# Kernel tuning notes

Hardware: AMD Instinct MI355X
Metric: run time of the kernel (lower is better)

Reference implementation:

```python
import jax, jax.numpy as jnp
import numpy as np

B, T, C = 1, 2048, 1024
H, KVH = 16, 4
D = C // H            # 64
KV = KVH * D          # 256
EPS = 1e-6
SCALE = 1.0 / np.sqrt(D)
ROPE_BASE = 10000.0


def setup_inputs() -> dict:
    key = jax.random.key(0)
    ks = jax.random.split(key, 8)
    s = 0.02
    return dict(
        x=jax.random.normal(ks[0], (B, T, C), jnp.float32),
        Wq=jax.random.normal(ks[1], (C, C), jnp.float32) * s,
        Wk=jax.random.normal(ks[2], (KV, C), jnp.float32) * s,
        Wv=jax.random.normal(ks[3], (KV, C), jnp.float32) * s,
        Wo=jax.random.normal(ks[4], (C, C), jnp.float32) * s,
        q_norm_w=jnp.ones((C,), jnp.float32),
        k_norm_w=jnp.ones((KV,), jnp.float32),
        fgate_w=jax.random.normal(ks[5], (H, C), jnp.float32) * s,
        fgate_b=jnp.zeros((H,), jnp.float32),
        weight_lambda=jax.random.normal(ks[6], (C, H), jnp.float32) * s,
    )


def _rmsnorm(x, w):
    var = jnp.mean(x * x, axis=-1, keepdims=True)
    return x * jax.lax.rsqrt(var + EPS) * w


def _rotate_half(x):
    x1, x2 = jnp.split(x, 2, axis=-1)
    return jnp.concatenate([-x2, x1], axis=-1)


def _apply_rope(q, k):
    # q: [B,H,T,D], k: [B,KVH,T,D]; position_ids = arange(T)
    inv_freq = 1.0 / (ROPE_BASE ** (jnp.arange(0, D, 2, dtype=jnp.float32) / D))
    freqs = jnp.outer(jnp.arange(T, dtype=jnp.float32), inv_freq)  # [T, D/2]
    emb = jnp.concatenate([freqs, freqs], axis=-1)                 # [T, D]
    cos = jnp.cos(emb)[None, None]                                  # [1,1,T,D]
    sin = jnp.sin(emb)[None, None]
    return q * cos + _rotate_half(q) * sin, k * cos + _rotate_half(k) * sin


def _forward(x, Wq, Wk, Wv, Wo, q_norm_w, k_norm_w, fgate_w, fgate_b, weight_lambda):
    q = _rmsnorm(x @ Wq.T, q_norm_w)          # [B,T,C]
    k = _rmsnorm(x @ Wk.T, k_norm_w)          # [B,T,KV]
    v = x @ Wv.T                              # [B,T,KV]
    q = q.reshape(B, T, H, D).transpose(0, 2, 1, 3)     # [B,H,T,D]
    k = k.reshape(B, T, KVH, D).transpose(0, 2, 1, 3)   # [B,KVH,T,D]
    v = v.reshape(B, T, KVH, D).transpose(0, 2, 1, 3)
    q, k = _apply_rope(q, k)
    # GQA: repeat_interleave kv heads
    g = H // KVH
    k = jnp.repeat(k, g, axis=1)              # [B,H,T,D]
    v = jnp.repeat(v, g, axis=1)
    # Forgetting gate (FoX): log f_t per head, with elu-based lambda scaling
    lam = jax.nn.elu(x @ weight_lambda) + 1.0            # [B,T,H]
    logit = (x @ fgate_w.T + fgate_b) * lam              # [B,T,H]
    log_f = (jax.nn.log_sigmoid(logit) / (lam + 1e-3)).transpose(0, 2, 1)  # [B,H,T]
    c = jnp.cumsum(log_f, axis=-1)                       # [B,H,T]
    bias = c[..., :, None] - c[..., None, :]             # [B,H,T,T]: sum_{t=j+1..i} log f_t
    scores = jnp.einsum('bhid,bhjd->bhij', q, k) * SCALE + bias
    causal = jnp.tril(jnp.ones((T, T), dtype=bool))
    scores = jnp.where(causal, scores, -jnp.inf)
    p = jax.nn.softmax(scores, axis=-1)
    y = jnp.einsum('bhij,bhjd->bhid', p, v)              # [B,H,T,D]
    y = y.transpose(0, 2, 1, 3).reshape(B, T, C)
    return y @ Wo.T


def reference(x, Wq, Wk, Wv, Wo, q_norm_w, k_norm_w, fgate_w, fgate_b, weight_lambda):
    return _forward(x, Wq, Wk, Wv, Wo, q_norm_w, k_norm_w, fgate_w, fgate_b, weight_lambda)
```

## Files before the change

kernel.cpp:

```cpp
#include <hip/hip_runtime.h>

typedef __bf16 bf16x8 __attribute__((ext_vector_type(8)));
typedef float f32x4 __attribute__((ext_vector_type(4)));

#define MFMA_BF16 __builtin_amdgcn_mfma_f32_16x16x32_bf16

static constexpr int T_ = 2048;
static constexpr int C_ = 1024;
static constexpr int H_ = 16;
static constexpr int KVH_ = 4;
static constexpr int D_ = 64;
static constexpr float SCALE_ = 0.125f;
static constexpr float MSHIFT_ = 10.0f;

__device__ inline void cvt8(__bf16* dst, const float* src) {
  float4 a = *(const float4*)src;
  float4 b = *(const float4*)(src + 4);
  bf16x8 r;
  r[0] = (__bf16)a.x; r[1] = (__bf16)a.y; r[2] = (__bf16)a.z; r[3] = (__bf16)a.w;
  r[4] = (__bf16)b.x; r[5] = (__bf16)b.y; r[6] = (__bf16)b.z; r[7] = (__bf16)b.w;
  *(bf16x8*)dst = r;
}

__global__ __launch_bounds__(256) void cvt_kernel(
    const float* __restrict__ x,  const float* __restrict__ wq,
    const float* __restrict__ wk, const float* __restrict__ wv,
    const float* __restrict__ wo, const float* __restrict__ wl,
    __bf16* __restrict__ xb,  __bf16* __restrict__ wqb,
    __bf16* __restrict__ wkb, __bf16* __restrict__ wvb,
    __bf16* __restrict__ wob, float* __restrict__ wlT)
{
  size_t i8 = ((size_t)blockIdx.x * 256 + threadIdx.x) * 8;
  if (i8 < 2097152)       cvt8(xb  + i8,            x  + i8);
  else if (i8 < 3145728)  cvt8(wqb + (i8-2097152),  wq + (i8-2097152));
  else if (i8 < 3407872)  cvt8(wkb + (i8-3145728),  wk + (i8-3145728));
  else if (i8 < 3670016)  cvt8(wvb + (i8-3407872),  wv + (i8-3407872));
  else if (i8 < 4718592)  cvt8(wob + (i8-3670016),  wo + (i8-3670016));
  else {
    size_t r = i8 - 4718592;
    if (r < 16384) {
#pragma unroll
      for (int j = 0; j < 8; ++j) {
        size_t idx = r + j;
        size_t hh = idx >> 10, c = idx & 1023;
        wlT[idx] = wl[c * 16 + hh];
      }
    }
  }
}

template <int BM>
__global__ __launch_bounds__(256) void gemm_bt_kernel(
    const __bf16* __restrict__ A, int K, int N,
    const __bf16* __restrict__ B0, int e0,
    const __bf16* __restrict__ B1, int e1,
    const __bf16* __restrict__ B2,
    float* __restrict__ outF)
{
  __shared__ __bf16 la[BM * 40];
  __shared__ __bf16 lb[128 * 40];
  const int m0 = blockIdx.y * BM;
  const int n0 = blockIdx.x * 128;
  const __bf16* Bs; int nrel;
  if (n0 < e0)      { Bs = B0; nrel = n0; }
  else if (n0 < e1) { Bs = B1; nrel = n0 - e0; }
  else              { Bs = B2; nrel = n0 - e1; }
  const int tid = threadIdx.x;
  const int arow = tid >> 2, acol = (tid & 3) * 8;
  const __bf16* ap = A  + (size_t)(m0   + arow) * K + acol;
  const __bf16* bp = Bs + (size_t)(nrel + arow) * K + acol;
  const int w = tid >> 6, lane = tid & 63, lq = lane >> 4, ln = lane & 15;
  const int wm = (w >> 1) * (BM / 2), wn = (w & 1) * 64;
  constexpr int FM = BM / 32;
  f32x4 acc[FM][4] = {};
  for (int k0 = 0; k0 < K; k0 += 32) {
    bf16x8 a0 = *(const bf16x8*)(ap + k0);
    bf16x8 a1{};
    if (BM == 128) a1 = *(const bf16x8*)(ap + (size_t)64 * K + k0);
    bf16x8 b0 = *(const bf16x8*)(bp + k0);
    bf16x8 b1 = *(const bf16x8*)(bp + (size_t)64 * K + k0);
    __syncthreads();
    *(bf16x8*)(la + arow * 40 + acol) = a0;
    if (BM == 128) *(bf16x8*)(la + (arow + 64) * 40 + acol) = a1;
    *(bf16x8*)(lb + arow * 40 + acol) = b0;
    *(bf16x8*)(lb + (arow + 64) * 40 + acol) = b1;
    __syncthreads();
    bf16x8 af[FM], bfr[4];
#pragma unroll
    for (int i = 0; i < FM; ++i)
      af[i] = *(const bf16x8*)(la + (wm + i * 16 + ln) * 40 + lq * 8);
#pragma unroll
    for (int j = 0; j < 4; ++j)
      bfr[j] = *(const bf16x8*)(lb + (wn + j * 16 + ln) * 40 + lq * 8);
#pragma unroll
    for (int i = 0; i < FM; ++i)
#pragma unroll
      for (int j = 0; j < 4; ++j)
        acc[i][j] = MFMA_BF16(af[i], bfr[j], acc[i][j], 0, 0, 0);
  }
#pragma unroll
  for (int i = 0; i < FM; ++i)
#pragma unroll
    for (int j = 0; j < 4; ++j)
#pragma unroll
      for (int r = 0; r < 4; ++r) {
        int row = m0 + wm + i * 16 + lq * 4 + r;
        int col = n0 + wn + j * 16 + ln;
        outF[(size_t)row * N + col] = acc[i][j][r];
      }
}

__global__ __launch_bounds__(256) void gates_kernel(
    const float* __restrict__ x, const float* __restrict__ fw,
    const float* __restrict__ fb, const float* __restrict__ wlT,
    float* __restrict__ logf)
{
  const int t = blockIdx.x;
  const int tid = threadIdx.x, w = tid >> 6, lane = tid & 63;
  float xv[16];
#pragma unroll
  for (int i = 0; i < 16; ++i)
    xv[i] = x[(size_t)t * C_ + i * 64 + lane];
#pragma unroll
  for (int u = 0; u < 4; ++u) {
    int h = w * 4 + u;
    float s1 = 0.f, s2 = 0.f;
#pragma unroll
    for (int i = 0; i < 16; ++i) {
      int cidx = i * 64 + lane;
      s1 += xv[i] * wlT[(size_t)h * C_ + cidx];
      s2 += xv[i] * fw[(size_t)h * C_ + cidx];
    }
    for (int m = 32; m; m >>= 1) {
      s1 += __shfl_xor(s1, m);
      s2 += __shfl_xor(s2, m);
    }
    if (lane == 0) {
      float lam = (s1 > 0.f ? s1 : expm1f(s1)) + 1.0f;
      float logit = (s2 + fb[h]) * lam;
      float ls = (logit >= 0.f) ? -log1pf(expf(-logit))
                                : (logit - log1pf(expf(logit)));
      logf[(size_t)h * T_ + t] = ls / (lam + 1e-3f);
    }
  }
}

__global__ __launch_bounds__(64) void cumsum_kernel(
    const float* __restrict__ logf, float* __restrict__ csum)
{
  const int h = blockIdx.x;
  const int lane = threadIdx.x;
  float carry = 0.f;
  for (int ch = 0; ch < T_ / 64; ++ch) {
    float v = logf[(size_t)h * T_ + ch * 64 + lane];
#pragma unroll
    for (int d = 1; d < 64; d <<= 1) {
      float tv = __shfl_up(v, d);
      if (lane >= d) v += tv;
    }
    v += carry;
    csum[(size_t)h * T_ + ch * 64 + lane] = v;
    carry = __shfl(v, 63);
  }
}

__global__ __launch_bounds__(256) void normrope_kernel(
    const float* __restrict__ qkv, const float* __restrict__ qw,
    const float* __restrict__ kw, __bf16* __restrict__ qh,
    __bf16* __restrict__ kh, __bf16* __restrict__ vh)
{
  const int t = blockIdx.x, tid = threadIdx.x;
  __shared__ float qn[1024];
  __shared__ float kn[256];
  __shared__ float red[16];
  __shared__ float rc[32], rs[32];
  if (tid < 32) {
    float fr = (float)t * exp2f((float)tid * -0.41524101186404527f);
    float sn, cs;
    sincosf(fr, &sn, &cs);
    rc[tid] = cs; rs[tid] = sn;
  }
  const float* row = qkv + (size_t)t * 1536;
  float4 q4 = *(const float4*)(row + tid * 4);
  float kvl = row[1024 + tid];
  float vvl = row[1280 + tid];
  float ssq = q4.x * q4.x + q4.y * q4.y + q4.z * q4.z + q4.w * q4.w;
  float ssk = kvl * kvl;
  const int lane = tid & 63, w = tid >> 6;
  for (int m = 32; m; m >>= 1) {
    ssq += __shfl_xor(ssq, m);
    ssk += __shfl_xor(ssk, m);
  }
  if (lane == 0) { red[w] = ssq; red[8 + w] = ssk; }
  __syncthreads();
  float sq = red[0] + red[1] + red[2] + red[3];
  float sk = red[8] + red[9] + red[10] + red[11];
  float rq = rsqrtf(sq * (1.0f / 1024.f) + 1e-6f);
  float rk = rsqrtf(sk * (1.0f / 256.f) + 1e-6f);
  qn[tid * 4 + 0] = q4.x * rq * qw[tid * 4 + 0];
  qn[tid * 4 + 1] = q4.y * rq * qw[tid * 4 + 1];
  qn[tid * 4 + 2] = q4.z * rq * qw[tid * 4 + 2];
  qn[tid * 4 + 3] = q4.w * rq * qw[tid * 4 + 3];
  kn[tid] = kvl * rk * kw[tid];
  __syncthreads();
#pragma unroll
  for (int u = 0; u < 4; ++u) {
    int cidx = tid * 4 + u;
    int hh = cidx >> 6, d = cidx & 63, i = d & 31;
    float cs = rc[i], sn = rs[i];
    float val = (d < 32) ? (qn[cidx] * cs - qn[cidx + 32] * sn)
                         : (qn[cidx] * cs + qn[cidx - 32] * sn);
    qh[(size_t)hh * T_ * D_ + (size_t)t * D_ + d] = (__bf16)val;
  }
  {
    int d = tid & 63, kvhh = tid >> 6, i = d & 31;
    float cs = rc[i], sn = rs[i];
    float kval = (d < 32) ? (kn[tid] * cs - kn[tid + 32] * sn)
                          : (kn[tid] * cs + kn[tid - 32] * sn);
    kh[(size_t)kvhh * T_ * D_ + (size_t)t * D_ + d] = (__bf16)kval;
    vh[(size_t)kvhh * T_ * D_ + (size_t)t * D_ + d] = (__bf16)vvl;
  }
}

__global__ __launch_bounds__(256) void vtrans_kernel(
    const __bf16* __restrict__ vh, __bf16* __restrict__ vt)
{
  const int tb = blockIdx.x, kvh = blockIdx.y;
  __shared__ __bf16 tile[64][72];
  const int tid = threadIdx.x;
  const int r = tid >> 2, cb = (tid & 3) * 16;
  const __bf16* src = vh + (size_t)kvh * T_ * D_ + (size_t)(tb * 64 + r) * D_ + cb;
  bf16x8 v0 = *(const bf16x8*)(src);
  bf16x8 v1 = *(const bf16x8*)(src + 8);
  *(bf16x8*)(&tile[r][cb]) = v0;
  *(bf16x8*)(&tile[r][cb + 8]) = v1;
  __syncthreads();
  bf16x8 o0, o1;
#pragma unroll
  for (int j = 0; j < 8; ++j) o0[j] = tile[cb + j][r];
#pragma unroll
  for (int j = 0; j < 8; ++j) o1[j] = tile[cb + 8 + j][r];
  __bf16* dst = vt + (size_t)kvh * D_ * T_ + (size_t)r * T_ + tb * 64 + cb;
  *(bf16x8*)(dst) = o0;
  *(bf16x8*)(dst + 8) = o1;
}

__global__ __launch_bounds__(256) void attn_kernel(
    const __bf16* __restrict__ qh, const __bf16* __restrict__ kh,
    const __bf16* __restrict__ vt, const float* __restrict__ csum,
    __bf16* __restrict__ y)
{
  const int ib = blockIdx.x, h = blockIdx.y;
  const int i0 = ib * 64, kvh = h >> 2;
  __shared__ __bf16 kt[64 * 72];
  __shared__ __bf16 vtt[64 * 72];
  __shared__ __bf16 pt[4][16 * 72];
  const int tid = threadIdx.x;
  const int w = tid >> 6, lane = tid & 63, lq = lane >> 4, ln = lane & 15;
  const int srow = tid >> 2, scol = (tid & 3) * 16;
  const __bf16* kbase = kh + (size_t)kvh * T_ * D_;
  const __bf16* vbase = vt + (size_t)kvh * D_ * T_;
  const __bf16* qp = qh + ((size_t)h * T_ + i0 + w * 16 + ln) * D_;
  bf16x8 aq0 = *(const bf16x8*)(qp + lq * 8);
  bf16x8 aq1 = *(const bf16x8*)(qp + 32 + lq * 8);
  float ci[4];
#pragma unroll
  for (int r = 0; r < 4; ++r)
    ci[r] = csum[(size_t)h * T_ + i0 + w * 16 + lq * 4 + r];
  f32x4 o[4] = {};
  f32x4 ls = {0.f, 0.f, 0.f, 0.f};
  bf16x8 ones;
#pragma unroll
  for (int j = 0; j < 8; ++j) ones[j] = (__bf16)1.0f;
  __bf16* pw = &pt[w][0];

  bf16x8 kr0 = *(const bf16x8*)(kbase + (size_t)srow * D_ + scol);
  bf16x8 kr1 = *(const bf16x8*)(kbase + (size_t)srow * D_ + scol + 8);
  bf16x8 vr0 = *(const bf16x8*)(vbase + (size_t)srow * T_ + scol);
  bf16x8 vr1 = *(const bf16x8*)(vbase + (size_t)srow * T_ + scol + 8);
  *(bf16x8*)(kt + srow * 72 + scol) = kr0;
  *(bf16x8*)(kt + srow * 72 + scol + 8) = kr1;
  *(bf16x8*)(vtt + srow * 72 + scol) = vr0;
  *(bf16x8*)(vtt + srow * 72 + scol + 8) = vr1;
  __syncthreads();

  auto tilebody = [&](int j0, bool diag) {
    f32x4 s[4];
    const f32x4 zf = {0.f, 0.f, 0.f, 0.f};
#pragma unroll
    for (int jj = 0; jj < 4; ++jj) {
      bf16x8 bk0 = *(const bf16x8*)(kt + (jj * 16 + ln) * 72 + lq * 8);
      bf16x8 bk1 = *(const bf16x8*)(kt + (jj * 16 + ln) * 72 + 32 + lq * 8);
      s[jj] = MFMA_BF16(aq0, bk0, zf, 0, 0, 0);
      s[jj] = MFMA_BF16(aq1, bk1, s[jj], 0, 0, 0);
    }
    float cj[4];
#pragma unroll
    for (int jj = 0; jj < 4; ++jj)
      cj[jj] = csum[(size_t)h * T_ + j0 + jj * 16 + ln];
#pragma unroll
    for (int jj = 0; jj < 4; ++jj)
#pragma unroll
      for (int r = 0; r < 4; ++r) {
        float arg = fmaf(s[jj][r], SCALE_, ci[r] - cj[jj] - MSHIFT_);
        float p = __expf(arg);
        if (diag && (jj * 16 + ln > w * 16 + lq * 4 + r)) p = 0.f;
        pw[(lq * 4 + r) * 72 + jj * 16 + ln] = (__bf16)p;
      }
    asm volatile("s_waitcnt lgkmcnt(0)" ::: "memory");
    bf16x8 pa0 = *(const bf16x8*)(pw + ln * 72 + lq * 8);
    bf16x8 pa1 = *(const bf16x8*)(pw + ln * 72 + 32 + lq * 8);
    ls = MFMA_BF16(pa0, ones, ls, 0, 0, 0);
    ls = MFMA_BF16(pa1, ones, ls, 0, 0, 0);
#pragma unroll
    for (int dd = 0; dd < 4; ++dd) {
      bf16x8 bv0 = *(const bf16x8*)(vtt + (dd * 16 + ln) * 72 + lq * 8);
      bf16x8 bv1 = *(const bf16x8*)(vtt + (dd * 16 + ln) * 72 + 32 + lq * 8);
      o[dd] = MFMA_BF16(pa0, bv0, o[dd], 0, 0, 0);
      o[dd] = MFMA_BF16(pa1, bv1, o[dd], 0, 0, 0);
    }
  };

  for (int jt = 0; jt < ib; ++jt) {
    const int j0n = (jt + 1) * 64;
    kr0 = *(const bf16x8*)(kbase + (size_t)(j0n + srow) * D_ + scol);
    kr1 = *(const bf16x8*)(kbase + (size_t)(j0n + srow) * D_ + scol + 8);
    vr0 = *(const bf16x8*)(vbase + (size_t)srow * T_ + j0n + scol);
    vr1 = *(const bf16x8*)(vbase + (size_t)srow * T_ + j0n + scol + 8);
    tilebody(jt * 64, false);
    __syncthreads();
    *(bf16x8*)(kt + srow * 72 + scol) = kr0;
    *(bf16x8*)(kt + srow * 72 + scol + 8) = kr1;
    *(bf16x8*)(vtt + srow * 72 + scol) = vr0;
    *(bf16x8*)(vtt + srow * 72 + scol + 8) = vr1;
    __syncthreads();
  }
  tilebody(i0, true);

#pragma unroll
  for (int dd = 0; dd < 4; ++dd)
#pragma unroll
    for (int r = 0; r < 4; ++r) {
      int iabs = i0 + w * 16 + lq * 4 + r;
      int col = h * 64 + dd * 16 + ln;
      y[(size_t)iabs * C_ + col] = (__bf16)(o[dd][r] / ls[r]);
    }
}

extern "C" void kernel_launch(void* const* d_in, const int* in_sizes, int n_in,
                              void* d_out, int out_size, void* d_ws, size_t ws_size,
                              hipStream_t stream) {
  const float* x   = (const float*)d_in[0];
  const float* Wq  = (const float*)d_in[1];
  const float* Wk  = (const float*)d_in[2];
  const float* Wv  = (const float*)d_in[3];
  const float* Wo  = (const float*)d_in[4];
  const float* qnw = (const float*)d_in[5];
  const float* knw = (const float*)d_in[6];
  const float* fgw = (const float*)d_in[7];
  const float* fgb = (const float*)d_in[8];
  const float* wl  = (const float*)d_in[9];

  char* ws = (char*)d_ws;
  size_t off = 0;
  float*  qkv  = (float*)(ws + off);  off += (size_t)T_ * 1536 * 4;
  float*  logf = (float*)(ws + off);  off += (size_t)H_ * T_ * 4;
  float*  csum = (float*)(ws + off);  off += (size_t)H_ * T_ * 4;
  __bf16* qh   = (__bf16*)(ws + off); off += (size_t)H_ * T_ * D_ * 2;
  __bf16* kh   = (__bf16*)(ws + off); off += (size_t)KVH_ * T_ * D_ * 2;
  __bf16* vh   = (__bf16*)(ws + off); off += (size_t)KVH_ * T_ * D_ * 2;
  __bf16* vt   = (__bf16*)(ws + off); off += (size_t)KVH_ * T_ * D_ * 2;
  __bf16* y    = (__bf16*)(ws + off); off += (size_t)T_ * C_ * 2;
  __bf16* xb   = (__bf16*)(ws + off); off += (size_t)T_ * C_ * 2;
  __bf16* wqb  = (__bf16*)(ws + off); off += (size_t)C_ * C_ * 2;
  __bf16* wkb  = (__bf16*)(ws + off); off += (size_t)256 * C_ * 2;
  __bf16* wvb  = (__bf16*)(ws + off); off += (size_t)256 * C_ * 2;
  __bf16* wob  = (__bf16*)(ws + off); off += (size_t)C_ * C_ * 2;
  float*  wlT  = (float*)(ws + off);  off += (size_t)H_ * C_ * 4;

  cvt_kernel<<<2312, 256, 0, stream>>>(x, Wq, Wk, Wv, Wo, wl,
                                       xb, wqb, wkb, wvb, wob, wlT);
  gemm_bt_kernel<64><<<dim3(12, 32), 256, 0, stream>>>(
      xb, 1024, 1536, wqb, 1024, wkb, 1280, wvb, qkv);
  gates_kernel<<<T_, 256, 0, stream>>>(x, fgw, fgb, wlT, logf);
  cumsum_kernel<<<H_, 64, 0, stream>>>(logf, csum);
  normrope_kernel<<<T_, 256, 0, stream>>>(qkv, qnw, knw, qh, kh, vh);
  vtrans_kernel<<<dim3(T_ / 64, KVH_), 256, 0, stream>>>(vh, vt);
  attn_kernel<<<dim3(T_ / 64, H_), 256, 0, stream>>>(qh, kh, vt, csum, y);
  gemm_bt_kernel<64><<<dim3(8, 32), 256, 0, stream>>>(
      y, 1024, 1024, wob, 1024, wob, 1024, wob, (float*)d_out);
}
```

Baseline: 204.3 us.

## Split causal attention over key chunks with a reduction pass; fuse gates into prep

```diff
diff --git a/kernel.cpp b/kernel.cpp
--- a/kernel.cpp
+++ b/kernel.cpp
@@ -22,29 +22,51 @@
   *(bf16x8*)dst = r;
 }
 
-__global__ __launch_bounds__(256) void cvt_kernel(
+__global__ __launch_bounds__(256) void prep_kernel(
     const float* __restrict__ x,  const float* __restrict__ wq,
     const float* __restrict__ wk, const float* __restrict__ wv,
-    const float* __restrict__ wo, const float* __restrict__ wl,
+    const float* __restrict__ wo, const float* __restrict__ fw,
+    const float* __restrict__ fb, const float* __restrict__ wl,
     __bf16* __restrict__ xb,  __bf16* __restrict__ wqb,
     __bf16* __restrict__ wkb, __bf16* __restrict__ wvb,
-    __bf16* __restrict__ wob, float* __restrict__ wlT)
-{
-  size_t i8 = ((size_t)blockIdx.x * 256 + threadIdx.x) * 8;
-  if (i8 < 2097152)       cvt8(xb  + i8,            x  + i8);
-  else if (i8 < 3145728)  cvt8(wqb + (i8-2097152),  wq + (i8-2097152));
-  else if (i8 < 3407872)  cvt8(wkb + (i8-3145728),  wk + (i8-3145728));
-  else if (i8 < 3670016)  cvt8(wvb + (i8-3407872),  wv + (i8-3407872));
-  else if (i8 < 4718592)  cvt8(wob + (i8-3670016),  wo + (i8-3670016));
-  else {
-    size_t r = i8 - 4718592;
-    if (r < 16384) {
-#pragma unroll
-      for (int j = 0; j < 8; ++j) {
-        size_t idx = r + j;
-        size_t hh = idx >> 10, c = idx & 1023;
-        wlT[idx] = wl[c * 16 + hh];
-      }
+    __bf16* __restrict__ wob, float* __restrict__ logf)
+{
+  const int bid = blockIdx.x;
+  if (bid < 2304) {
+    size_t i8 = ((size_t)bid * 256 + threadIdx.x) * 8;
+    if (i8 < 2097152)       cvt8(xb  + i8,            x  + i8);
+    else if (i8 < 3145728)  cvt8(wqb + (i8-2097152),  wq + (i8-2097152));
+    else if (i8 < 3407872)  cvt8(wkb + (i8-3145728),  wk + (i8-3145728));
+    else if (i8 < 3670016)  cvt8(wvb + (i8-3407872),  wv + (i8-3407872));
+    else                    cvt8(wob + (i8-3670016),  wo + (i8-3670016));
+    return;
+  }
+  const int t = bid - 2304;
+  const int tid = threadIdx.x, w = tid >> 6, lane = tid & 63;
+  float xv[16];
+#pragma unroll
+  for (int i = 0; i < 16; ++i)
+    xv[i] = x[(size_t)t * C_ + i * 64 + lane];
+#pragma unroll
+  for (int u = 0; u < 4; ++u) {
+    int h = w * 4 + u;
+    float s1 = 0.f, s2 = 0.f;
+#pragma unroll
+    for (int i = 0; i < 16; ++i) {
+      int cidx = i * 64 + lane;
+      s1 += xv[i] * wl[(size_t)cidx * H_ + h];
+      s2 += xv[i] * fw[(size_t)h * C_ + cidx];
+    }
+    for (int m = 32; m; m >>= 1) {
+      s1 += __shfl_xor(s1, m);
+      s2 += __shfl_xor(s2, m);
+    }
+    if (lane == 0) {
+      float lam = (s1 > 0.f ? s1 : expm1f(s1)) + 1.0f;
+      float logit = (s2 + fb[h]) * lam;
+      float ls = (logit >= 0.f) ? -log1pf(expf(-logit))
+                                : (logit - log1pf(expf(logit)));
+      logf[(size_t)h * T_ + t] = ls / (lam + 1e-3f);
     }
   }
 }
@@ -110,41 +132,6 @@
       }
 }
 
-__global__ __launch_bounds__(256) void gates_kernel(
-    const float* __restrict__ x, const float* __restrict__ fw,
-    const float* __restrict__ fb, const float* __restrict__ wlT,
-    float* __restrict__ logf)
-{
-  const int t = blockIdx.x;
-  const int tid = threadIdx.x, w = tid >> 6, lane = tid & 63;
-  float xv[16];
-#pragma unroll
-  for (int i = 0; i < 16; ++i)
-    xv[i] = x[(size_t)t * C_ + i * 64 + lane];
-#pragma unroll
-  for (int u = 0; u < 4; ++u) {
-    int h = w * 4 + u;
-    float s1 = 0.f, s2 = 0.f;
-#pragma unroll
-    for (int i = 0; i < 16; ++i) {
-      int cidx = i * 64 + lane;
-      s1 += xv[i] * wlT[(size_t)h * C_ + cidx];
-      s2 += xv[i] * fw[(size_t)h * C_ + cidx];
-    }
-    for (int m = 32; m; m >>= 1) {
-      s1 += __shfl_xor(s1, m);
-      s2 += __shfl_xor(s2, m);
-    }
-    if (lane == 0) {
-      float lam = (s1 > 0.f ? s1 : expm1f(s1)) + 1.0f;
-      float logit = (s2 + fb[h]) * lam;
-      float ls = (logit >= 0.f) ? -log1pf(expf(-logit))
-                                : (logit - log1pf(expf(logit)));
-      logf[(size_t)h * T_ + t] = ls / (lam + 1e-3f);
-    }
-  }
-}
-
 __global__ __launch_bounds__(64) void cumsum_kernel(
     const float* __restrict__ logf, float* __restrict__ csum)
 {
@@ -245,12 +232,15 @@
   *(bf16x8*)(dst + 8) = o1;
 }
 
-__global__ __launch_bounds__(256) void attn_kernel(
+__global__ __launch_bounds__(256) void attn_part_kernel(
     const __bf16* __restrict__ qh, const __bf16* __restrict__ kh,
     const __bf16* __restrict__ vt, const float* __restrict__ csum,
-    __bf16* __restrict__ y)
-{
-  const int ib = blockIdx.x, h = blockIdx.y;
+    float* __restrict__ po, float* __restrict__ pls)
+{
+  const int ib = blockIdx.x, h = blockIdx.y, z = blockIdx.z;
+  const int jbeg = z * 8;
+  if (jbeg > ib) return;
+  const int jend = min(jbeg + 8, ib + 1);
   const int i0 = ib * 64, kvh = h >> 2;
   __shared__ __bf16 kt[64 * 72];
   __shared__ __bf16 vtt[64 * 72];
@@ -274,10 +264,10 @@
   for (int j = 0; j < 8; ++j) ones[j] = (__bf16)1.0f;
   __bf16* pw = &pt[w][0];
 
-  bf16x8 kr0 = *(const bf16x8*)(kbase + (size_t)srow * D_ + scol);
-  bf16x8 kr1 = *(const bf16x8*)(kbase + (size_t)srow * D_ + scol + 8);
-  bf16x8 vr0 = *(const bf16x8*)(vbase + (size_t)srow * T_ + scol);
-  bf16x8 vr1 = *(const bf16x8*)(vbase + (size_t)srow * T_ + scol + 8);
+  bf16x8 kr0 = *(const bf16x8*)(kbase + (size_t)(jbeg * 64 + srow) * D_ + scol);
+  bf16x8 kr1 = *(const bf16x8*)(kbase + (size_t)(jbeg * 64 + srow) * D_ + scol + 8);
+  bf16x8 vr0 = *(const bf16x8*)(vbase + (size_t)srow * T_ + jbeg * 64 + scol);
+  bf16x8 vr1 = *(const bf16x8*)(vbase + (size_t)srow * T_ + jbeg * 64 + scol + 8);
   *(bf16x8*)(kt + srow * 72 + scol) = kr0;
   *(bf16x8*)(kt + srow * 72 + scol + 8) = kr1;
   *(bf16x8*)(vtt + srow * 72 + scol) = vr0;
@@ -321,7 +311,7 @@
     }
   };
 
-  for (int jt = 0; jt < ib; ++jt) {
+  for (int jt = jbeg; jt < jend - 1; ++jt) {
     const int j0n = (jt + 1) * 64;
     kr0 = *(const bf16x8*)(kbase + (size_t)(j0n + srow) * D_ + scol);
     kr1 = *(const bf16x8*)(kbase + (size_t)(j0n + srow) * D_ + scol + 8);
@@ -335,16 +325,48 @@
     *(bf16x8*)(vtt + srow * 72 + scol + 8) = vr1;
     __syncthreads();
   }
-  tilebody(i0, true);
-
+  tilebody((jend - 1) * 64, (jend - 1) == ib);
+
+  const size_t pbase = ((size_t)(h * 32 + ib) * 4 + z) * 4096;
+  const size_t lbase = ((size_t)(h * 32 + ib) * 4 + z) * 64;
 #pragma unroll
   for (int dd = 0; dd < 4; ++dd)
 #pragma unroll
     for (int r = 0; r < 4; ++r) {
-      int iabs = i0 + w * 16 + lq * 4 + r;
-      int col = h * 64 + dd * 16 + ln;
-      y[(size_t)iabs * C_ + col] = (__bf16)(o[dd][r] / ls[r]);
-    }
+      int row = w * 16 + lq * 4 + r;
+      int col = dd * 16 + ln;
+      po[pbase + row * 64 + col] = o[dd][r];
+    }
+  if (ln == 0)
+#pragma unroll
+    for (int r = 0; r < 4; ++r)
+      pls[lbase + w * 16 + lq * 4 + r] = ls[r];
+}
+
+__global__ __launch_bounds__(256) void attn_red_kernel(
+    const float* __restrict__ po, const float* __restrict__ pls,
+    __bf16* __restrict__ y)
+{
+  const int ib = blockIdx.x, h = blockIdx.y;
+  const int nch = ib / 8 + 1;
+  const int tid = threadIdx.x;
+  __shared__ float lss[64];
+  const size_t pbase = (size_t)(h * 32 + ib) * 4 * 4096;
+  const size_t lbase = (size_t)(h * 32 + ib) * 4 * 64;
+  if (tid < 64) {
+    float s = 0.f;
+    for (int c = 0; c < nch; ++c) s += pls[lbase + c * 64 + tid];
+    lss[tid] = s;
+  }
+  __syncthreads();
+#pragma unroll 4
+  for (int u = 0; u < 16; ++u) {
+    int idx = u * 256 + tid;
+    int row = idx >> 6, col = idx & 63;
+    float acc = 0.f;
+    for (int c = 0; c < nch; ++c) acc += po[pbase + c * 4096 + idx];
+    y[(size_t)(ib * 64 + row) * C_ + h * 64 + col] = (__bf16)(acc / lss[row]);
+  }
 }
 
 extern "C" void kernel_launch(void* const* d_in, const int* in_sizes, int n_in,
@@ -364,6 +386,12 @@
   char* ws = (char*)d_ws;
   size_t off = 0;
   float*  qkv  = (float*)(ws + off);  off += (size_t)T_ * 1536 * 4;
+  __bf16* xb   = (__bf16*)(ws + off); off += (size_t)T_ * C_ * 2;
+  __bf16* wqb  = (__bf16*)(ws + off); off += (size_t)C_ * C_ * 2;
+  __bf16* wkb  = (__bf16*)(ws + off); off += (size_t)256 * C_ * 2;
+  __bf16* wvb  = (__bf16*)(ws + off); off += (size_t)256 * C_ * 2;
+  float*  po   = (float*)ws;
+  off = (size_t)16 * 32 * 4 * 4096 * 4;
   float*  logf = (float*)(ws + off);  off += (size_t)H_ * T_ * 4;
   float*  csum = (float*)(ws + off);  off += (size_t)H_ * T_ * 4;
   __bf16* qh   = (__bf16*)(ws + off); off += (size_t)H_ * T_ * D_ * 2;
@@ -371,22 +399,18 @@
   __bf16* vh   = (__bf16*)(ws + off); off += (size_t)KVH_ * T_ * D_ * 2;
   __bf16* vt   = (__bf16*)(ws + off); off += (size_t)KVH_ * T_ * D_ * 2;
   __bf16* y    = (__bf16*)(ws + off); off += (size_t)T_ * C_ * 2;
-  __bf16* xb   = (__bf16*)(ws + off); off += (size_t)T_ * C_ * 2;
-  __bf16* wqb  = (__bf16*)(ws + off); off += (size_t)C_ * C_ * 2;
-  __bf16* wkb  = (__bf16*)(ws + off); off += (size_t)256 * C_ * 2;
-  __bf16* wvb  = (__bf16*)(ws + off); off += (size_t)256 * C_ * 2;
   __bf16* wob  = (__bf16*)(ws + off); off += (size_t)C_ * C_ * 2;
-  float*  wlT  = (float*)(ws + off);  off += (size_t)H_ * C_ * 4;
-
-  cvt_kernel<<<2312, 256, 0, stream>>>(x, Wq, Wk, Wv, Wo, wl,
-                                       xb, wqb, wkb, wvb, wob, wlT);
+  float*  pls  = (float*)(ws + off);  off += (size_t)16 * 32 * 4 * 64 * 4;
+
+  prep_kernel<<<4352, 256, 0, stream>>>(x, Wq, Wk, Wv, Wo, fgw, fgb, wl,
+                                        xb, wqb, wkb, wvb, wob, logf);
   gemm_bt_kernel<64><<<dim3(12, 32), 256, 0, stream>>>(
       xb, 1024, 1536, wqb, 1024, wkb, 1280, wvb, qkv);
-  gates_kernel<<<T_, 256, 0, stream>>>(x, fgw, fgb, wlT, logf);
   cumsum_kernel<<<H_, 64, 0, stream>>>(logf, csum);
   normrope_kernel<<<T_, 256, 0, stream>>>(qkv, qnw, knw, qh, kh, vh);
   vtrans_kernel<<<dim3(T_ / 64, KVH_), 256, 0, stream>>>(vh, vt);
-  attn_kernel<<<dim3(T_ / 64, H_), 256, 0, stream>>>(qh, kh, vt, csum, y);
+  attn_part_kernel<<<dim3(32, 16, 4), 256, 0, stream>>>(qh, kh, vt, csum, po, pls);
+  attn_red_kernel<<<dim3(32, 16), 256, 0, stream>>>(po, pls, y);
   gemm_bt_kernel<64><<<dim3(8, 32), 256, 0, stream>>>(
       y, 1024, 1024, wob, 1024, wob, 1024, wob, (float*)d_out);
 }
```

Measured after the change: 267.9 us. 1.31x slower.
